# Performance work log

Hardware: AMD Instinct MI355X
Metric: run time of the kernel (lower is better)

Reference implementation:

```python
import jax, jax.numpy as jnp
import numpy as np

RES = 32          # resolution (32, 32) -> N = 1024 tokens
HEADS = 16
EMB = 1024
BATCH = 8
N = RES * RES


def _bias_idxs(res):
    # relative-offset index table, [N, N] with values in [0, res*res)
    coords = np.stack(np.meshgrid(np.arange(res), np.arange(res), indexing='ij'), -1).reshape(-1, 2)
    d = np.abs(coords[:, None, :] - coords[None, :, :])  # [N, N, 2]
    return jnp.asarray(d[..., 0] * res + d[..., 1], dtype=jnp.int64)


def setup_inputs() -> dict:
    key = jax.random.key(0)
    k1, k2, k3, k4, k5 = jax.random.split(key, 5)
    x = jax.random.normal(k1, (BATCH, N, EMB), dtype=jnp.float32)
    w_qkv = jax.random.normal(k2, (3 * EMB, EMB), dtype=jnp.float32) * 0.02
    biases = jax.random.normal(k3, (HEADS, RES * RES), dtype=jnp.float32) * 0.02
    bias_idxs = _bias_idxs(RES)
    w_out = jax.random.normal(k4, (EMB, EMB), dtype=jnp.float32) * 0.02
    b_out = jax.random.normal(k5, (EMB,), dtype=jnp.float32) * 0.02
    return {"x": x, "w_qkv": w_qkv, "biases": biases,
            "bias_idxs": bias_idxs, "w_out": w_out, "b_out": b_out}


def reference(x, w_qkv, biases, bias_idxs, w_out, b_out):
    b, n, e = x.shape
    h = HEADS
    d = e // h
    scale = d ** -0.5
    # to_qkv: Linear(e, 3e, bias=False); torch Linear computes x @ W.T
    qkv = x @ w_qkv.T                                   # [b, n, 3e]
    q, k, v = jnp.split(qkv, 3, axis=-1)
    def to_heads(t):
        return t.reshape(b, n, h, d).transpose(0, 2, 1, 3)  # b h n d
    q, k, v = to_heads(q), to_heads(k), to_heads(v)
    scores = jnp.einsum('bhid,bhjd->bhij', q, k) * scale    # [b, h, n, n]
    scores = scores + biases[:, bias_idxs]                  # gather -> [h, n, n], broadcast over b
    attn = jax.nn.softmax(scores, axis=-1)
    out = jnp.einsum('bhij,bhjd->bhid', attn, v)            # [b, h, n, d]
    out = out.transpose(0, 2, 1, 3).reshape(b, n, e)        # b n (h d)
    # to_out: Linear(e, e) with bias (dropout = identity at inference)
    return out @ w_out.T + b_out
```

## Files before the change

kernel.cpp:

```cpp
#include <hip/hip_runtime.h>
#include <stdint.h>


#define LOG2E 1.4426950408889634f
#define QSCL 0.18033688011112042f

typedef __attribute__((ext_vector_type(8))) short short8;
typedef __attribute__((ext_vector_type(4))) short short4v;
typedef __attribute__((ext_vector_type(4))) float floatx4;
typedef __attribute__((ext_vector_type(2))) unsigned int uint2v;
typedef __attribute__((ext_vector_type(4))) unsigned int uint4v;

__device__ __forceinline__ short f2bf(float f) {
  uint32_t u = __builtin_bit_cast(uint32_t, f);
  u = (u + 0x7FFFu + ((u >> 16) & 1u)) >> 16;
  return (short)(uint16_t)u;
}
__device__ __forceinline__ float bf2f(short s) {
  uint32_t u = ((uint32_t)(uint16_t)s) << 16;
  return __builtin_bit_cast(float, u);
}
__device__ __forceinline__ float fast_exp2(float x) {
#if __has_builtin(__builtin_amdgcn_exp2f)
  return __builtin_amdgcn_exp2f(x);
#else
  return exp2f(x);
#endif
}

__device__ __forceinline__ void gload_lds16(const short* g, short* l) {
  __builtin_amdgcn_global_load_lds(
      (const __attribute__((address_space(1))) void*)g,
      (__attribute__((address_space(3))) void*)l, 16, 0, 0);
}

__global__ void prep(const float* __restrict__ x, const float* __restrict__ wqkv,
                     const float* __restrict__ wout, const float* __restrict__ biases,
                     short* __restrict__ xb, short* __restrict__ wqkvb,
                     short* __restrict__ woutb, short* __restrict__ biast) {
  int blk = blockIdx.x, tid = threadIdx.x;
  if (blk < 12288) {
    const float* src;
    short* dst;
    int i;
    if (blk < 8192) { src = x; dst = xb; i = blk * 256 + tid; }
    else if (blk < 11264) { src = wqkv; dst = wqkvb; i = (blk - 8192) * 256 + tid; }
    else { src = wout; dst = woutb; i = (blk - 11264) * 256 + tid; }
    float4 f = ((const float4*)src)[i];
    short4v o;
    o.x = f2bf(f.x); o.y = f2bf(f.y); o.z = f2bf(f.z); o.w = f2bf(f.w);
    ((short4v*)dst)[i] = o;
  } else {
    int tile = (blk - 12288) * 4 + (tid >> 6);
    int lane = tid & 63, qd = lane >> 4, col = lane & 15;
    int bp = tile & 1, ap = (tile >> 1) & 1, dra = (tile >> 2) & 31, h = tile >> 7;
    int ci = 16 * bp + col;
    short4v o;
#pragma unroll
    for (int r = 0; r < 4; r++) {
      int cj = 16 * ap + 4 * qd + r;
      int dc = cj - ci; if (dc < 0) dc = -dc;
      o[r] = f2bf(biases[h * 1024 + dra * 32 + dc] * LOG2E);
    }
    *(short4v*)&biast[(size_t)tile * 256 + lane * 4] = o;
  }
}

template <int MODE>
__global__ __launch_bounds__(256, 3) void gemm_bt(
    const short* __restrict__ A, const short* __restrict__ Bt,
    short* __restrict__ qo, short* __restrict__ ko, short* __restrict__ vto,
    const float* __restrict__ bvec, float* __restrict__ outf) {
  __shared__ __align__(16) short sA[128 * 64];
  __shared__ __align__(16) short sB[128 * 64];
  const int tid = threadIdx.x;
  const int w = tid >> 6, lane = tid & 63;
  const int wr = w >> 1, wc = w & 1;
  const int bm = blockIdx.y, bn = blockIdx.x;
  const int qd = lane >> 4, col = lane & 15;

  floatx4 acc[4][4] = {};
  const int rowA0 = bm * 128, rowB0 = bn * 128;
  const int ciw = w * 256;

  for (int kk = 0; kk < 1024; kk += 64) {
    __syncthreads();
#pragma unroll
    for (int n = 0; n < 4; n++) {
      int ci = ciw + n * 64 + lane;
      int r = ci >> 3, c = (ci & 7) ^ (r & 7);
      gload_lds16(A + (size_t)(rowA0 + r) * 1024 + kk + c * 8, &sA[ci * 8]);
    }
#pragma unroll
    for (int n = 0; n < 4; n++) {
      int ci = ciw + n * 64 + lane;
      int r = ci >> 3, c = (ci & 7) ^ (r & 7);
      gload_lds16(Bt + (size_t)(rowB0 + r) * 1024 + kk + c * 8, &sB[ci * 8]);
    }
    __syncthreads();

#pragma unroll
    for (int ks = 0; ks < 2; ks++) {
      const int ch = qd + ks * 4;
      short8 af[4], bff[4];
#pragma unroll
      for (int rt = 0; rt < 4; rt++) {
        int r = wr * 64 + rt * 16 + col;
        af[rt] = *(const short8*)&sA[r * 64 + ((ch ^ (r & 7)) << 3)];
      }
#pragma unroll
      for (int ct = 0; ct < 4; ct++) {
        int r = wc * 64 + ct * 16 + col;
        bff[ct] = *(const short8*)&sB[r * 64 + ((ch ^ (r & 7)) << 3)];
      }
#pragma unroll
      for (int rt = 0; rt < 4; rt++)
#pragma unroll
        for (int ct = 0; ct < 4; ct++)
          acc[rt][ct] = __builtin_amdgcn_mfma_f32_16x16x32_bf16(af[rt], bff[ct], acc[rt][ct], 0, 0, 0);
    }
  }

  if (MODE == 0) {
    if (bn >= 16) {
#pragma unroll
      for (int rt = 0; rt < 4; rt++) {
#pragma unroll
        for (int ct = 0; ct < 4; ct++) {
          int Cg = bn * 128 + wc * 64 + ct * 16 + col;
          int e = Cg & 1023, h = e >> 6, dd = e & 63;
          short4v pv;
#pragma unroll
          for (int r = 0; r < 4; r++) pv[r] = f2bf(acc[rt][ct][r]);
          int R0 = bm * 128 + wr * 64 + rt * 16 + qd * 4;
          int b = R0 >> 10, n0 = R0 & 1023;
          int bh = b * 16 + h;
          *(short4v*)&vto[((size_t)bh * 64 + dd) * 1024 + n0] = pv;
        }
      }
    } else {
#pragma unroll
      for (int rt = 0; rt < 4; rt++) {
#pragma unroll
        for (int ct = 0; ct < 4; ct++) {
          int Cg = bn * 128 + wc * 64 + ct * 16 + col;
          int which = Cg >> 10, e = Cg & 1023, h = e >> 6, dd = e & 63;
#pragma unroll
          for (int r = 0; r < 4; r++) {
            int R = bm * 128 + wr * 64 + rt * 16 + qd * 4 + r;
            int b = R >> 10, n = R & 1023;
            int bh = b * 16 + h;
            float av = acc[rt][ct][r];
            if (which == 0) av *= QSCL;
            short v = f2bf(av);
            if (which == 0)
              qo[((size_t)bh * 1024 + n) * 64 + dd] = v;
            else
              ko[((size_t)bh * 1024 + n) * 64 + dd] = v;
          }
        }
      }
    }
  } else {
#pragma unroll
    for (int rt = 0; rt < 4; rt++)
#pragma unroll
      for (int ct = 0; ct < 4; ct++) {
        int Cg = bn * 128 + wc * 64 + ct * 16 + col;
        float bo = bvec[Cg];
#pragma unroll
        for (int r = 0; r < 4; r++) {
          int R = bm * 128 + wr * 64 + rt * 16 + qd * 4 + r;
          outf[(size_t)R * 1024 + Cg] = acc[rt][ct][r] + bo;
        }
      }
  }
}

__global__ __launch_bounds__(256, 3) void attn_fused(
    const short* __restrict__ q, const short* __restrict__ k,
    const short* __restrict__ vt, const short* __restrict__ biast,
    short* __restrict__ ao) {
  __shared__ __align__(16) short smem[20480];
  short* sQ = smem;
  short* sK = smem + 4096;
  short* sVt = smem + 12288;
  const int tid = threadIdx.x, w = tid >> 6, lane = tid & 63;
  const int bh = blockIdx.x, qt = blockIdx.y;
  const int h = bh & 15;
  const int qd = lane >> 4, col = lane & 15;
  const short* qb = q + (size_t)bh * 65536;
  const short* kb = k + (size_t)bh * 65536;
  const short* vb = vt + (size_t)bh * 65536;
  const int ciw = w * 256;

#pragma unroll
  for (int n = 0; n < 2; n++) {
    int ci = w * 128 + n * 64 + lane;
    int r = ci >> 3, c = (ci & 7) ^ (r & 7);
    gload_lds16(qb + (size_t)(qt * 64 + r) * 64 + c * 8, &sQ[ci * 8]);
  }

  floatx4 oacc[4][4] = {};
  float rs[4] = {0.f, 0.f, 0.f, 0.f};

  for (int js = 0; js < 8; js++) {
#pragma unroll
    for (int n = 0; n < 4; n++) {
      int ci = ciw + n * 64 + lane;
      int r = ci >> 3, c = (ci & 7) ^ (r & 7);
      gload_lds16(kb + (size_t)(js * 128 + r) * 64 + c * 8, &sK[ci * 8]);
    }
#pragma unroll
    for (int n = 0; n < 4; n++) {
      int ci = ciw + n * 64 + lane;
      int r = ci >> 4, c = (ci & 15) ^ (r & 15);
      gload_lds16(vb + (size_t)r * 1024 + js * 128 + c * 8, &sVt[ci * 8]);
    }
    __syncthreads();

    uint32_t pw[4][4];
#pragma unroll
    for (int rt = 0; rt < 2; rt++) {
      const int a = js * 8 + w * 2 + rt;
      const int ar = a >> 1, ap = a & 1;
      short4v bfrag[4];
#pragma unroll
      for (int ct = 0; ct < 4; ct++) {
        int b = qt * 4 + ct;
        int dra = ar - (b >> 1); if (dra < 0) dra = -dra;
        int tile = ((h * 32 + dra) * 2 + ap) * 2 + (b & 1);
        bfrag[ct] = *(const short4v*)&biast[(size_t)tile * 256 + lane * 4];
      }
      const int r = w * 32 + rt * 16 + col;
      floatx4 sacc[4];
#pragma unroll
      for (int ct = 0; ct < 4; ct++) {
        sacc[ct][0] = bf2f(bfrag[ct][0]);
        sacc[ct][1] = bf2f(bfrag[ct][1]);
        sacc[ct][2] = bf2f(bfrag[ct][2]);
        sacc[ct][3] = bf2f(bfrag[ct][3]);
      }
      __builtin_amdgcn_s_setprio(1);
#pragma unroll
      for (int ks = 0; ks < 2; ks++) {
        const int ch = qd + ks * 4;
        short8 ak = *(const short8*)&sK[r * 64 + ((ch ^ (r & 7)) << 3)];
        short8 bqf[4];
#pragma unroll
        for (int ct = 0; ct < 4; ct++) {
          int r2 = ct * 16 + col;
          bqf[ct] = *(const short8*)&sQ[r2 * 64 + ((ch ^ (r2 & 7)) << 3)];
        }
#pragma unroll
        for (int ct = 0; ct < 4; ct++)
          sacc[ct] = __builtin_amdgcn_mfma_f32_16x16x32_bf16(ak, bqf[ct], sacc[ct], 0, 0, 0);
      }
      __builtin_amdgcn_s_setprio(0);
#pragma unroll
      for (int ct = 0; ct < 4; ct++) {
        float e0 = fast_exp2(sacc[ct][0]);
        float e1 = fast_exp2(sacc[ct][1]);
        float e2 = fast_exp2(sacc[ct][2]);
        float e3 = fast_exp2(sacc[ct][3]);
        rs[ct] += (e0 + e1) + (e2 + e3);
        uint32_t u0 = __builtin_bit_cast(uint32_t, e0) + 0x8000u;
        uint32_t u1 = __builtin_bit_cast(uint32_t, e1) + 0x8000u;
        uint32_t u2 = __builtin_bit_cast(uint32_t, e2) + 0x8000u;
        uint32_t u3 = __builtin_bit_cast(uint32_t, e3) + 0x8000u;
        pw[ct][2 * rt + 0] = __builtin_amdgcn_perm(u1, u0, 0x07060302u);
        pw[ct][2 * rt + 1] = __builtin_amdgcn_perm(u3, u2, 0x07060302u);
      }
    }

    short8 pa[4], bv[4];
#pragma unroll
    for (int ct = 0; ct < 4; ct++)
      pa[ct] = __builtin_bit_cast(short8, (uint4v){pw[ct][0], pw[ct][1], pw[ct][2], pw[ct][3]});
    const int jc0 = 4 * w + (qd >> 1), off = 4 * (qd & 1);
#pragma unroll
    for (int ct = 0; ct < 4; ct++) {
      int d = ct * 16 + col;
      short4v lo4 = *(const short4v*)&sVt[d * 128 + ((jc0 ^ (d & 15)) << 3) + off];
      short4v hi4 = *(const short4v*)&sVt[d * 128 + (((jc0 + 2) ^ (d & 15)) << 3) + off];
      bv[ct] = __builtin_shufflevector(lo4, hi4, 0, 1, 2, 3, 4, 5, 6, 7);
    }
    __builtin_amdgcn_s_setprio(1);
#pragma unroll
    for (int ci2 = 0; ci2 < 4; ci2++)
#pragma unroll
      for (int cd = 0; cd < 4; cd++)
        oacc[ci2][cd] = __builtin_amdgcn_mfma_f32_16x16x32_bf16(pa[ci2], bv[cd], oacc[ci2][cd], 0, 0, 0);
    __builtin_amdgcn_s_setprio(0);
    __syncthreads();
  }

  float* fs = (float*)smem;
#pragma unroll
  for (int ct = 0; ct < 4; ct++)
    fs[(w * 4 + qd) * 64 + 16 * ct + col] = rs[ct];
  __syncthreads();
  {
    float tot = 0.f;
#pragma unroll
    for (int kk = 0; kk < 16; kk++) tot += fs[kk * 64 + lane];
    fs[1024 + lane] = 1.0f / tot;
  }
  __syncthreads();
  float myinv[8];
  if (w < 2) {
#pragma unroll
    for (int t2 = 0; t2 < 2; t2++)
#pragma unroll
      for (int r = 0; r < 4; r++)
        myinv[t2 * 4 + r] = fs[1024 + (w * 2 + t2) * 16 + 4 * qd + r];
  }
  __syncthreads();
  if (w >= 2) {
    float* ob = fs + (w - 2) * 4096;
#pragma unroll
    for (int ci2 = 0; ci2 < 4; ci2++)
#pragma unroll
      for (int cd = 0; cd < 4; cd++)
        *(floatx4*)&ob[((ci2 * 4 + cd) * 64 + lane) * 4] = oacc[ci2][cd];
  }
  __syncthreads();
  if (w < 2) {
    float* ob = fs + w * 4096;
#pragma unroll
    for (int ci2 = 0; ci2 < 4; ci2++)
#pragma unroll
      for (int cd = 0; cd < 4; cd++)
        oacc[ci2][cd] += *(const floatx4*)&ob[((ci2 * 4 + cd) * 64 + lane) * 4];
  }
  __syncthreads();
  if (w == 1) {
#pragma unroll
    for (int t2 = 0; t2 < 2; t2++)
#pragma unroll
      for (int cd = 0; cd < 4; cd++)
        *(floatx4*)&fs[((t2 * 4 + cd) * 64 + lane) * 4] = oacc[t2][cd];
  }
  if (w == 0) {
#pragma unroll
    for (int t2 = 0; t2 < 2; t2++)
#pragma unroll
      for (int cd = 0; cd < 4; cd++)
        *(floatx4*)&fs[2048 + ((t2 * 4 + cd) * 64 + lane) * 4] = oacc[2 + t2][cd];
  }
  __syncthreads();
  const int b = bh >> 4;
  if (w == 0) {
#pragma unroll
    for (int t2 = 0; t2 < 2; t2++) {
#pragma unroll
      for (int cd = 0; cd < 4; cd++) {
        floatx4 p = *(const floatx4*)&fs[((t2 * 4 + cd) * 64 + lane) * 4];
        floatx4 o = (t2 == 0 ? oacc[0][cd] : oacc[1][cd]);
        o += p;
#pragma unroll
        for (int r = 0; r < 4; r++) {
          int i = 16 * t2 + 4 * qd + r;
          int n = qt * 64 + i;
          int dd = cd * 16 + col;
          ao[(((size_t)b * 1024 + n) << 10) + h * 64 + dd] = f2bf(o[r] * myinv[t2 * 4 + r]);
        }
      }
    }
  } else if (w == 1) {
#pragma unroll
    for (int t2 = 0; t2 < 2; t2++) {
#pragma unroll
      for (int cd = 0; cd < 4; cd++) {
        floatx4 p = *(const floatx4*)&fs[2048 + ((t2 * 4 + cd) * 64 + lane) * 4];
        floatx4 o = (t2 == 0 ? oacc[2][cd] : oacc[3][cd]);
        o += p;
#pragma unroll
        for (int r = 0; r < 4; r++) {
          int i = 16 * (2 + t2) + 4 * qd + r;
          int n = qt * 64 + i;
          int dd = cd * 16 + col;
          ao[(((size_t)b * 1024 + n) << 10) + h * 64 + dd] = f2bf(o[r] * myinv[t2 * 4 + r]);
        }
      }
    }
  }
}

extern "C" void kernel_launch(void* const* d_in, const int* in_sizes, int n_in,
                              void* d_out, int out_size, void* d_ws, size_t ws_size,
                              hipStream_t stream) {
  const float* x = (const float*)d_in[0];
  const float* w_qkv = (const float*)d_in[1];
  const float* biases = (const float*)d_in[2];
  const float* w_out = (const float*)d_in[4];
  const float* b_out = (const float*)d_in[5];
  float* out = (float*)d_out;

  char* ws = (char*)d_ws;
  short* xb    = (short*)(ws + 0);
  short* wqkvb = (short*)(ws + 16777216);
  short* woutb = (short*)(ws + 23068672);
  short* qb    = (short*)(ws + 25165824);
  short* kb    = (short*)(ws + 41943040);
  short* vtb   = (short*)(ws + 58720256);
  short* aob   = (short*)(ws + 75497472);
  short* biast = (short*)(ws + 92274688);

  prep<<<13312, 256, 0, stream>>>(x, w_qkv, w_out, biases, xb, wqkvb, woutb, biast);
  gemm_bt<0><<<dim3(24, 64), 256, 0, stream>>>(xb, wqkvb, qb, kb, vtb, nullptr, nullptr);
  attn_fused<<<dim3(128, 16), 256, 0, stream>>>(qb, kb, vtb, biast, aob);
  gemm_bt<1><<<dim3(8, 64), 256, 0, stream>>>(aob, woutb, nullptr, nullptr, nullptr, b_out, out);
}
```

Measured before the change: 248.4 us.

## Load K and V fragments directly from global memory, dropping LDS staging

```diff
diff --git a/kernel.cpp b/kernel.cpp
--- a/kernel.cpp
+++ b/kernel.cpp
@@ -181,10 +181,8 @@
     const short* __restrict__ q, const short* __restrict__ k,
     const short* __restrict__ vt, const short* __restrict__ biast,
     short* __restrict__ ao) {
-  __shared__ __align__(16) short smem[20480];
+  __shared__ __align__(16) short smem[16384];
   short* sQ = smem;
-  short* sK = smem + 4096;
-  short* sVt = smem + 12288;
   const int tid = threadIdx.x, w = tid >> 6, lane = tid & 63;
   const int bh = blockIdx.x, qt = blockIdx.y;
   const int h = bh & 15;
@@ -192,7 +190,6 @@
   const short* qb = q + (size_t)bh * 65536;
   const short* kb = k + (size_t)bh * 65536;
   const short* vb = vt + (size_t)bh * 65536;
-  const int ciw = w * 256;
 
 #pragma unroll
   for (int n = 0; n < 2; n++) {
@@ -200,24 +197,15 @@
     int r = ci >> 3, c = (ci & 7) ^ (r & 7);
     gload_lds16(qb + (size_t)(qt * 64 + r) * 64 + c * 8, &sQ[ci * 8]);
   }
+  __syncthreads();
 
   floatx4 oacc[4][4] = {};
   float rs[4] = {0.f, 0.f, 0.f, 0.f};
 
   for (int js = 0; js < 8; js++) {
-#pragma unroll
-    for (int n = 0; n < 4; n++) {
-      int ci = ciw + n * 64 + lane;
-      int r = ci >> 3, c = (ci & 7) ^ (r & 7);
-      gload_lds16(kb + (size_t)(js * 128 + r) * 64 + c * 8, &sK[ci * 8]);
-    }
-#pragma unroll
-    for (int n = 0; n < 4; n++) {
-      int ci = ciw + n * 64 + lane;
-      int r = ci >> 4, c = (ci & 15) ^ (r & 15);
-      gload_lds16(vb + (size_t)r * 1024 + js * 128 + c * 8, &sVt[ci * 8]);
-    }
-    __syncthreads();
+    int qoff = 0;
+    asm volatile("" : "+v"(qoff));
+    const short* sQp = sQ + qoff;
 
     uint32_t pw[4][4];
 #pragma unroll
@@ -232,7 +220,9 @@
         int tile = ((h * 32 + dra) * 2 + ap) * 2 + (b & 1);
         bfrag[ct] = *(const short4v*)&biast[(size_t)tile * 256 + lane * 4];
       }
-      const int r = w * 32 + rt * 16 + col;
+      const short* krow = kb + (size_t)(js * 128 + w * 32 + rt * 16 + col) * 64;
+      short8 ak0 = *(const short8*)(krow + qd * 8);
+      short8 ak1 = *(const short8*)(krow + qd * 8 + 32);
       floatx4 sacc[4];
 #pragma unroll
       for (int ct = 0; ct < 4; ct++) {
@@ -245,12 +235,12 @@
 #pragma unroll
       for (int ks = 0; ks < 2; ks++) {
         const int ch = qd + ks * 4;
-        short8 ak = *(const short8*)&sK[r * 64 + ((ch ^ (r & 7)) << 3)];
+        short8 ak = (ks == 0) ? ak0 : ak1;
         short8 bqf[4];
 #pragma unroll
         for (int ct = 0; ct < 4; ct++) {
           int r2 = ct * 16 + col;
-          bqf[ct] = *(const short8*)&sQ[r2 * 64 + ((ch ^ (r2 & 7)) << 3)];
+          bqf[ct] = *(const short8*)&sQp[r2 * 64 + ((ch ^ (r2 & 7)) << 3)];
         }
 #pragma unroll
         for (int ct = 0; ct < 4; ct++)
@@ -277,12 +267,11 @@
 #pragma unroll
     for (int ct = 0; ct < 4; ct++)
       pa[ct] = __builtin_bit_cast(short8, (uint4v){pw[ct][0], pw[ct][1], pw[ct][2], pw[ct][3]});
-    const int jc0 = 4 * w + (qd >> 1), off = 4 * (qd & 1);
 #pragma unroll
     for (int ct = 0; ct < 4; ct++) {
-      int d = ct * 16 + col;
-      short4v lo4 = *(const short4v*)&sVt[d * 128 + ((jc0 ^ (d & 15)) << 3) + off];
-      short4v hi4 = *(const short4v*)&sVt[d * 128 + (((jc0 + 2) ^ (d & 15)) << 3) + off];
+      const short* vrow = vb + (size_t)(ct * 16 + col) * 1024 + js * 128 + 32 * w + 4 * qd;
+      short4v lo4 = *(const short4v*)vrow;
+      short4v hi4 = *(const short4v*)(vrow + 16);
       bv[ct] = __builtin_shufflevector(lo4, hi4, 0, 1, 2, 3, 4, 5, 6, 7);
     }
     __builtin_amdgcn_s_setprio(1);
@@ -292,8 +281,9 @@
       for (int cd = 0; cd < 4; cd++)
         oacc[ci2][cd] = __builtin_amdgcn_mfma_f32_16x16x32_bf16(pa[ci2], bv[cd], oacc[ci2][cd], 0, 0, 0);
     __builtin_amdgcn_s_setprio(0);
-    __syncthreads();
-  }
+  }
+
+  __syncthreads();
 
   float* fs = (float*)smem;
 #pragma unroll
```

Measured after the change: 296.9 us. +19.5%, slower.
